# Optimization experiments

Measured on AMD Instinct MI355X. Metric: run time of the kernel, lower is better.

## Reference

```python
import jax, jax.numpy as jnp
import numpy as np

B, L, D_MODEL = 8, 1024, 1024
NUM_HEADS, QUERY_GROUPS = 16, 4
HEAD_DIM = D_MODEL // NUM_HEADS          # 64
HEADS_PER_GROUP = NUM_HEADS // QUERY_GROUPS
ROPE_THETA = 10000.0
QK_NORM_EPS = 1e-10
QKV_OUT = NUM_HEADS * HEAD_DIM + 2 * QUERY_GROUPS * HEAD_DIM  # 1536


def setup_inputs() -> dict:
    key = jax.random.key(0)
    k1, k2, k3 = jax.random.split(key, 3)
    x = jax.random.normal(k1, (B, L, D_MODEL), dtype=jnp.float32)
    w_qkv = jax.random.normal(k2, (QKV_OUT, D_MODEL), dtype=jnp.float32) * 0.02
    w_o = jax.random.normal(k3, (D_MODEL, D_MODEL), dtype=jnp.float32) * 0.02
    return {"x": x, "w_qkv": w_qkv, "w_o": w_o, "H_patch": 32, "W_patch": 32}


def _qk_norm(t, eps=QK_NORM_EPS):
    # L2 normalize over head_dim (qk_norm_type=2)
    return t / (jnp.linalg.norm(t, axis=-1, keepdims=True) + eps)


def _rope2d(t, H, W):
    # t: [B, L, nh, hd] with L == H*W
    b, _, nh, hd = t.shape
    inv_freq = 1.0 / ROPE_THETA ** (jnp.arange(0, hd, 2, dtype=jnp.float32) / hd)  # [hd/2]
    pos_h = jnp.arange(H, dtype=jnp.float32)
    pos_w = jnp.arange(W, dtype=jnp.float32)
    # additive combination of H and W frequencies: [H, W, hd/2]
    freqs = pos_h[:, None, None] * inv_freq + pos_w[None, :, None] * inv_freq
    cos = jnp.cos(freqs)[None, :, :, None, :]  # [1,H,W,1,hd/2]
    sin = jnp.sin(freqs)[None, :, :, None, :]
    ts = t.reshape(b, H, W, nh, hd)
    x1, x2 = ts[..., ::2], ts[..., 1::2]
    rot = jnp.concatenate([x1 * cos - x2 * sin, x1 * sin + x2 * cos], axis=-1)
    return rot.reshape(b, H * W, nh, hd)


def reference(x, w_qkv, w_o, H_patch, W_patch):
    b, l, _ = x.shape
    qkv = jnp.einsum('bld,ed->ble', x, w_qkv)  # [B, L, QKV_OUT]
    q, k, v = jnp.split(qkv, [NUM_HEADS * HEAD_DIM, NUM_HEADS * HEAD_DIM + QUERY_GROUPS * HEAD_DIM], axis=-1)
    q = q.reshape(b, l, NUM_HEADS, HEAD_DIM)
    k = k.reshape(b, l, QUERY_GROUPS, HEAD_DIM)
    v = v.reshape(b, l, QUERY_GROUPS, HEAD_DIM)
    # QK norm (use_qk_norm=True default)
    q = _qk_norm(q)
    k = _qk_norm(k)
    # 2D RoPE
    q = _rope2d(q, H_patch, W_patch)
    k = _rope2d(k, H_patch, W_patch)
    # GQA head expansion (use_mqa=False): repeat_interleave along head dim
    k = jnp.repeat(k, HEADS_PER_GROUP, axis=2)
    v = jnp.repeat(v, HEADS_PER_GROUP, axis=2)
    # [B, nh, L, hd]
    q = q.transpose(0, 2, 1, 3)
    k = k.transpose(0, 2, 1, 3)
    v = v.transpose(0, 2, 1, 3)
    # SDPA with default scale (softmax_scale arg is ignored by the original code);
    # padding_mask=None path: attn_mask ends up None, so no causal mask either.
    scale = 1.0 / jnp.sqrt(jnp.float32(HEAD_DIM))
    scores = jnp.einsum('bhqd,bhkd->bhqk', q, k) * scale
    attn = jax.nn.softmax(scores, axis=-1)
    out = jnp.einsum('bhqk,bhkd->bhqd', attn, v)
    out = out.transpose(0, 2, 1, 3).reshape(b, l, D_MODEL)
    return jnp.einsum('bld,ed->ble', out, w_o)
```

## Files before the change

kernel.cpp:

```cpp
#include <hip/hip_runtime.h>
#include <hip/hip_bf16.h>
#include <cstdint>
#include <cstddef>


typedef __bf16 bf16x8 __attribute__((ext_vector_type(8)));
typedef __bf16 bf16x4 __attribute__((ext_vector_type(4)));
typedef float floatx4 __attribute__((ext_vector_type(4)));
typedef uint32_t u32x2 __attribute__((ext_vector_type(2)));
typedef uint32_t u32x4 __attribute__((ext_vector_type(4)));

typedef unsigned int u32_g __attribute__((address_space(1)));
typedef unsigned int u32_l __attribute__((address_space(3)));

__device__ __forceinline__ void gl_lds16(const void* g, void* l) {
  __builtin_amdgcn_global_load_lds((const u32_g*)g, (u32_l*)l, 16, 0, 0);
}

constexpr int CH = 520;
__device__ __forceinline__ int pidx(int r, int k) {
  return (r >> 3) * CH + (r & 7) * 64 + k;
}

#define LOG2_THETA 13.287712379549449f

__global__ __launch_bounds__(256)
void cvt_all(const float* __restrict__ x, const float* __restrict__ wq,
             const float* __restrict__ wo, __bf16* __restrict__ out) {
  int i = blockIdx.x * 256 + threadIdx.x;
  float4 v;
  if (i < 2097152)      v = ((const float4*)x)[i];
  else if (i < 2490368) v = ((const float4*)wq)[i - 2097152];
  else                  v = ((const float4*)wo)[i - 2490368];
  bf16x4 o = {(__bf16)v.x, (__bf16)v.y, (__bf16)v.z, (__bf16)v.w};
  ((bf16x4*)out)[i] = o;
}

__global__ __launch_bounds__(256, 2)
void gemm_qkv(const __bf16* __restrict__ A, const __bf16* __restrict__ Bw,
              __bf16* __restrict__ Q, __bf16* __restrict__ Ko,
              __bf16* __restrict__ Vt, const int* __restrict__ Wp) {
  __shared__ __align__(16) __bf16 sAB[32 * CH];
  __bf16* sA = sAB;
  __bf16* sB = sAB + 16 * CH;
  const int tid = threadIdx.x, wave = tid >> 6, lane = tid & 63;
  const int quad = lane >> 4, lm = lane & 15;
  const int bm = blockIdx.x / 12, bn = blockIdx.x % 12;
  const int wm = wave & 1, wn = wave >> 1;
  const int rowA0 = bm << 7, rowB0 = bn << 7;
  const int lr = lane >> 3, lc = (lane & 7) * 8;

  floatx4 acc[4][4] = {};

  for (int k0 = 0; k0 < 1024; k0 += 64) {
    __syncthreads();
    for (int j = 0; j < 4; ++j) {
      int c = wave * 4 + j;
      gl_lds16(A + (size_t)(rowA0 + c * 8 + lr) * 1024 + k0 + lc, sA + c * CH);
      gl_lds16(Bw + (size_t)(rowB0 + c * 8 + lr) * 1024 + k0 + lc, sB + c * CH);
    }
    __syncthreads();
    for (int kb = 0; kb < 64; kb += 32) {
      const int ko = kb + quad * 8;
      bf16x8 af[4], bfv[4];
      for (int t = 0; t < 4; ++t) {
        af[t]  = *(const bf16x8*)(sA + pidx(wm * 64 + t * 16 + lm, ko));
        bfv[t] = *(const bf16x8*)(sB + pidx(wn * 64 + t * 16 + lm, ko));
      }
      for (int mt = 0; mt < 4; ++mt)
        for (int nt = 0; nt < 4; ++nt)
          acc[mt][nt] = __builtin_amdgcn_mfma_f32_16x16x32_bf16(af[mt], bfv[nt],
                                                                acc[mt][nt], 0, 0, 0);
    }
  }

  __syncthreads();

  const int hc = bn * 2 + wn;
  const int row0 = rowA0 + wm * 64;
  const int bb = row0 >> 10, l0 = row0 & 1023;

  if (hc < 20) {
    const bool isq = hc < 16;
    const int W = Wp[0];
    const float invfA = exp2f(-(float)lm * 0.03125f * LOG2_THETA);
    const float invfB = exp2f(-(float)(lm + 16) * 0.03125f * LOG2_THETA);
    __bf16* base = isq
        ? Q + (((size_t)bb * 16 + hc) * 1024 + l0) * 64
        : Ko + (((size_t)bb * 4 + (hc - 16)) * 1024 + l0) * 64;
    const int srcA = (lane & 48) | ((2 * lm) & 15);
    const bool lo = lm < 8;
    for (int mt = 0; mt < 4; ++mt)
      for (int r = 0; r < 4; ++r) {
        float a0 = acc[mt][0][r], a1 = acc[mt][1][r];
        float a2 = acc[mt][2][r], a3 = acc[mt][3][r];
        float ss = a0 * a0 + a1 * a1 + a2 * a2 + a3 * a3;
        ss += __shfl_xor(ss, 1); ss += __shfl_xor(ss, 2);
        ss += __shfl_xor(ss, 4); ss += __shfl_xor(ss, 8);
        float rn = (isq ? 0.125f : 1.0f) / (sqrtf(ss) + 1e-10f);
        a0 *= rn; a1 *= rn; a2 *= rn; a3 *= rn;
        float e0 = __shfl(a0, srcA),     e1 = __shfl(a1, srcA);
        float f0 = __shfl(a0, srcA + 1), f1 = __shfl(a1, srcA + 1);
        float g0 = __shfl(a2, srcA),     g1 = __shfl(a3, srcA);
        float h0 = __shfl(a2, srcA + 1), h1 = __shfl(a3, srcA + 1);
        float x1A = lo ? e0 : e1, x2A = lo ? f0 : f1;
        float x1B = lo ? g0 : g1, x2B = lo ? h0 : h1;
        int lrow = l0 + mt * 16 + quad * 4 + r;
        int pos = lrow / W + lrow % W;
        float fA = (float)pos * invfA, fB = (float)pos * invfB;
        float cA = __cosf(fA), sA_ = __sinf(fA);
        float cB = __cosf(fB), sB_ = __sinf(fB);
        __bf16* dst = base + (size_t)(mt * 16 + quad * 4 + r) * 64;
        dst[lm]      = (__bf16)(x1A * cA - x2A * sA_);
        dst[lm + 16] = (__bf16)(x1B * cB - x2B * sB_);
        dst[lm + 32] = (__bf16)(x1A * sA_ + x2A * cA);
        dst[lm + 48] = (__bf16)(x1B * sB_ + x2B * cB);
      }
  } else {
    const int g = hc - 20;
    __bf16* sT = sAB + wave * 4160;
    for (int mt = 0; mt < 4; ++mt)
      for (int nt = 0; nt < 4; ++nt)
        for (int r = 0; r < 4; ++r)
          sT[(mt * 16 + quad * 4 + r) * 65 + nt * 16 + lm] =
              (__bf16)acc[mt][nt][r];
    for (int pp = 0; pp < 8; ++pp) {
      int d = pp * 8 + (lane >> 3);
      int lloc = (lane & 7) * 8;
      bf16x8 o;
      for (int j = 0; j < 8; ++j) o[j] = sT[(lloc + j) * 65 + d];
      *(bf16x8*)(Vt + (((size_t)bb * 4 + g) * 64 + d) * 1024 + l0 + lloc) = o;
    }
  }
}

__global__ __launch_bounds__(256, 2)
void gemm_bt(const __bf16* __restrict__ A, const __bf16* __restrict__ B,
             float* __restrict__ Cf, int M, int N, int K) {
  __shared__ __align__(16) __bf16 sA[16 * CH];
  __shared__ __align__(16) __bf16 sB[16 * CH];
  const int tid = threadIdx.x;
  const int wave = tid >> 6, lane = tid & 63;
  const int ntiles = N >> 7;
  const int bm = blockIdx.x / ntiles, bn = blockIdx.x % ntiles;
  const int wm = wave & 1, wn = wave >> 1;
  const int rowA0 = bm << 7, rowB0 = bn << 7;
  const int lr = lane >> 3;
  const int lc = (lane & 7) * 8;

  floatx4 acc[4][4] = {};

  for (int k0 = 0; k0 < K; k0 += 64) {
    __syncthreads();
    for (int j = 0; j < 4; ++j) {
      int c = wave * 4 + j;
      gl_lds16(A + (size_t)(rowA0 + c * 8 + lr) * K + k0 + lc, sA + c * CH);
      gl_lds16(B + (size_t)(rowB0 + c * 8 + lr) * K + k0 + lc, sB + c * CH);
    }
    __syncthreads();
    for (int kb = 0; kb < 64; kb += 32) {
      const int ko = kb + (lane >> 4) * 8;
      bf16x8 af[4], bfv[4];
      for (int t = 0; t < 4; ++t) {
        af[t]  = *(const bf16x8*)(sA + pidx(wm * 64 + t * 16 + (lane & 15), ko));
        bfv[t] = *(const bf16x8*)(sB + pidx(wn * 64 + t * 16 + (lane & 15), ko));
      }
      for (int mt = 0; mt < 4; ++mt)
        for (int nt = 0; nt < 4; ++nt)
          acc[mt][nt] = __builtin_amdgcn_mfma_f32_16x16x32_bf16(af[mt], bfv[nt],
                                                                acc[mt][nt], 0, 0, 0);
    }
  }
  for (int mt = 0; mt < 4; ++mt)
    for (int nt = 0; nt < 4; ++nt)
      for (int r = 0; r < 4; ++r) {
        int row = rowA0 + wm * 64 + mt * 16 + (lane >> 4) * 4 + r;
        int col = rowB0 + wn * 64 + nt * 16 + (lane & 15);
        Cf[(size_t)row * N + col] = acc[mt][nt][r];
      }
}

__global__ __launch_bounds__(256, 4)
void flash(const __bf16* __restrict__ Q, const __bf16* __restrict__ K,
           const __bf16* __restrict__ Vt, __bf16* __restrict__ Oout) {
  __shared__ __align__(16) __bf16 sKV[16384];
  __shared__ float sL[128];
  const int tid = threadIdx.x, wave = tid >> 6, lane = tid & 63;
  const int quad = lane >> 4, lm = lane & 15;
  const int qt = blockIdx.x & 7, h = (blockIdx.x >> 3) & 15, b = blockIdx.x >> 7;
  const int g = h >> 2;
  const __bf16* Qb = Q + (((size_t)b * 16 + h) * 1024 + qt * 128) * 64;
  const __bf16* Kb = K + ((size_t)b * 4 + g) * 1024 * 64;
  const __bf16* Vb = Vt + ((size_t)b * 4 + g) * 64 * 1024;

  const int r8 = lane >> 3, gsw = (lane & 7) ^ r8;

  for (int j = 0; j < 4; ++j) {
    int c = wave * 4 + j;
    gl_lds16(Qb + (size_t)(c * 8 + r8) * 64 + gsw * 8, sKV + c * 512);
  }
  __syncthreads();
  bf16x8 qf[2][2];
  for (int mt = 0; mt < 2; ++mt)
    for (int hh = 0; hh < 2; ++hh) {
      int r = wave * 32 + mt * 16 + lm;
      qf[mt][hh] = *(const bf16x8*)(sKV + (r >> 3) * 512 + (r & 7) * 64 +
                                    (((hh * 4 + quad) ^ (r & 7)) * 8));
    }

  float l_acc[2] = {0.f, 0.f};
  floatx4 accO[2][4] = {};

  for (int kt = 0; kt < 8; ++kt) {
    __syncthreads();
    {
      int half = wave & 1;
      if (wave < 2) {
        for (int c = 0; c < 8; ++c)
          gl_lds16(Kb + (size_t)(kt * 128 + half * 64 + c * 8 + r8) * 64 + gsw * 8,
                   sKV + half * 4096 + c * 512);
      } else {
        for (int c = 0; c < 8; ++c)
          gl_lds16(Vb + (size_t)(c * 8 + r8) * 1024 + kt * 128 + half * 64 + gsw * 8,
                   sKV + 8192 + half * 4096 + c * 512);
      }
    }
    __syncthreads();

    for (int half = 0; half < 2; ++half) {
      const __bf16* sK = sKV + half * 4096;
      const __bf16* sV = sKV + 8192 + half * 4096;

      floatx4 accT[4][2] = {};
      for (int hh = 0; hh < 2; ++hh) {
        bf16x8 kf[4];
        for (int nt = 0; nt < 4; ++nt) {
          int r = nt * 16 + lm;
          kf[nt] = *(const bf16x8*)(sK + (r >> 3) * 512 + (r & 7) * 64 +
                                    (((hh * 4 + quad) ^ (r & 7)) * 8));
        }
        for (int nt = 0; nt < 4; ++nt)
          for (int mt = 0; mt < 2; ++mt)
            accT[nt][mt] = __builtin_amdgcn_mfma_f32_16x16x32_bf16(
                kf[nt], qf[mt][hh], accT[nt][mt], 0, 0, 0);
      }

      bf16x8 pf[2][2];
      for (int nt = 0; nt < 4; ++nt)
        for (int mt = 0; mt < 2; ++mt)
          for (int r = 0; r < 4; ++r) {
            float y = accT[nt][mt][r];
            float p = fmaf(y, fmaf(y, 0.5f, 1.0f), 1.0f);
            l_acc[mt] += p;
            pf[nt >> 1][mt][(nt & 1) * 4 + r] = (__bf16)p;
          }

      for (int hh = 0; hh < 2; ++hh)
        for (int dt = 0; dt < 4; ++dt) {
          int r = dt * 16 + lm;
          int rowoff = (r >> 3) * 512 + (r & 7) * 64;
          int lgA = hh * 4 + (quad >> 1);
          u32x2 vA = *(const u32x2*)(sV + rowoff + ((lgA ^ (r & 7)) * 8) + (quad & 1) * 4);
          u32x2 vB = *(const u32x2*)(sV + rowoff + (((lgA + 2) ^ (r & 7)) * 8) + (quad & 1) * 4);
          u32x4 vw = {vA[0], vA[1], vB[0], vB[1]};
          bf16x8 vf = __builtin_bit_cast(bf16x8, vw);
          for (int mt = 0; mt < 2; ++mt)
            accO[mt][dt] = __builtin_amdgcn_mfma_f32_16x16x32_bf16(
                pf[hh][mt], vf, accO[mt][dt], 0, 0, 0);
        }
    }
  }

  for (int mt = 0; mt < 2; ++mt) {
    float l = l_acc[mt];
    l += __shfl_xor(l, 16);
    l += __shfl_xor(l, 32);
    if (quad == 0) sL[wave * 32 + mt * 16 + lm] = l;
  }
  __syncthreads();

  for (int mt = 0; mt < 2; ++mt)
    for (int r = 0; r < 4; ++r) {
      float inv = 1.f / sL[wave * 32 + mt * 16 + quad * 4 + r];
      int row = qt * 128 + wave * 32 + mt * 16 + quad * 4 + r;
      for (int dt = 0; dt < 4; ++dt) {
        int col = dt * 16 + lm;
        Oout[((size_t)b * 1024 + row) * 1024 + h * 64 + col] =
            (__bf16)(accO[mt][dt][r] * inv);
      }
    }
}

extern "C" void kernel_launch(void* const* d_in, const int* in_sizes, int n_in,
                              void* d_out, int out_size, void* d_ws, size_t ws_size,
                              hipStream_t stream) {
  const float* x     = (const float*)d_in[0];
  const float* w_qkv = (const float*)d_in[1];
  const float* w_o   = (const float*)d_in[2];
  const int*   Wp    = (const int*)d_in[4];
  float* out = (float*)d_out;
  char* ws = (char*)d_ws;

  __bf16* xb    = (__bf16*)(ws + 0);
  __bf16* attn  = (__bf16*)(ws + 0);
  __bf16* wqkvb = (__bf16*)(ws + 16777216);
  __bf16* wob   = (__bf16*)(ws + 19922944);
  __bf16* Qb    = (__bf16*)(ws + 22020096);
  __bf16* Kb    = (__bf16*)(ws + 38797312);
  __bf16* Vtb   = (__bf16*)(ws + 42991616);

  cvt_all<<<10752, 256, 0, stream>>>(x, w_qkv, w_o, (__bf16*)ws);

  gemm_qkv<<<64 * 12, 256, 0, stream>>>(xb, wqkvb, Qb, Kb, Vtb, Wp);

  flash<<<1024, 256, 0, stream>>>(Qb, Kb, Vtb, attn);

  gemm_bt<<<64 * 8, 256, 0, stream>>>(attn, wob, out, 8192, 1024, 1024);
}
```

Measured before the change: 213.4 us.

## Enlarge flash query tile to 256 rows and use rotation-swizzled LDS layouts

```diff
diff --git a/kernel.cpp b/kernel.cpp
--- a/kernel.cpp
+++ b/kernel.cpp
@@ -17,9 +17,8 @@
   __builtin_amdgcn_global_load_lds((const u32_g*)g, (u32_l*)l, 16, 0, 0);
 }
 
-constexpr int CH = 520;
-__device__ __forceinline__ int pidx(int r, int k) {
-  return (r >> 3) * CH + (r & 7) * 64 + k;
+__device__ __forceinline__ int fidx8(int row, int g) {
+  return (row * 8 + ((g + row) & 7)) * 8;
 }
 
 #define LOG2_THETA 13.287712379549449f
@@ -40,15 +39,16 @@
 void gemm_qkv(const __bf16* __restrict__ A, const __bf16* __restrict__ Bw,
               __bf16* __restrict__ Q, __bf16* __restrict__ Ko,
               __bf16* __restrict__ Vt, const int* __restrict__ Wp) {
-  __shared__ __align__(16) __bf16 sAB[32 * CH];
+  __shared__ __align__(16) __bf16 sAB[16640];
   __bf16* sA = sAB;
-  __bf16* sB = sAB + 16 * CH;
+  __bf16* sB = sAB + 8192;
   const int tid = threadIdx.x, wave = tid >> 6, lane = tid & 63;
   const int quad = lane >> 4, lm = lane & 15;
   const int bm = blockIdx.x / 12, bn = blockIdx.x % 12;
   const int wm = wave & 1, wn = wave >> 1;
   const int rowA0 = bm << 7, rowB0 = bn << 7;
-  const int lr = lane >> 3, lc = (lane & 7) * 8;
+  const int r8 = lane >> 3;
+  const int gg = ((lane & 7) - r8) & 7;
 
   floatx4 acc[4][4] = {};
 
@@ -56,16 +56,16 @@
     __syncthreads();
     for (int j = 0; j < 4; ++j) {
       int c = wave * 4 + j;
-      gl_lds16(A + (size_t)(rowA0 + c * 8 + lr) * 1024 + k0 + lc, sA + c * CH);
-      gl_lds16(Bw + (size_t)(rowB0 + c * 8 + lr) * 1024 + k0 + lc, sB + c * CH);
+      gl_lds16(A + (size_t)(rowA0 + c * 8 + r8) * 1024 + k0 + gg * 8, sA + c * 512);
+      gl_lds16(Bw + (size_t)(rowB0 + c * 8 + r8) * 1024 + k0 + gg * 8, sB + c * 512);
     }
     __syncthreads();
     for (int kb = 0; kb < 64; kb += 32) {
-      const int ko = kb + quad * 8;
+      const int gk = (kb >> 3) + quad;
       bf16x8 af[4], bfv[4];
       for (int t = 0; t < 4; ++t) {
-        af[t]  = *(const bf16x8*)(sA + pidx(wm * 64 + t * 16 + lm, ko));
-        bfv[t] = *(const bf16x8*)(sB + pidx(wn * 64 + t * 16 + lm, ko));
+        af[t]  = *(const bf16x8*)(sA + fidx8(wm * 64 + t * 16 + lm, gk));
+        bfv[t] = *(const bf16x8*)(sB + fidx8(wn * 64 + t * 16 + lm, gk));
       }
       for (int mt = 0; mt < 4; ++mt)
         for (int nt = 0; nt < 4; ++nt)
@@ -137,16 +137,16 @@
 __global__ __launch_bounds__(256, 2)
 void gemm_bt(const __bf16* __restrict__ A, const __bf16* __restrict__ B,
              float* __restrict__ Cf, int M, int N, int K) {
-  __shared__ __align__(16) __bf16 sA[16 * CH];
-  __shared__ __align__(16) __bf16 sB[16 * CH];
+  __shared__ __align__(16) __bf16 sA[8192];
+  __shared__ __align__(16) __bf16 sB[8192];
   const int tid = threadIdx.x;
   const int wave = tid >> 6, lane = tid & 63;
   const int ntiles = N >> 7;
   const int bm = blockIdx.x / ntiles, bn = blockIdx.x % ntiles;
   const int wm = wave & 1, wn = wave >> 1;
   const int rowA0 = bm << 7, rowB0 = bn << 7;
-  const int lr = lane >> 3;
-  const int lc = (lane & 7) * 8;
+  const int r8 = lane >> 3;
+  const int gg = ((lane & 7) - r8) & 7;
 
   floatx4 acc[4][4] = {};
 
@@ -154,16 +154,16 @@
     __syncthreads();
     for (int j = 0; j < 4; ++j) {
       int c = wave * 4 + j;
-      gl_lds16(A + (size_t)(rowA0 + c * 8 + lr) * K + k0 + lc, sA + c * CH);
-      gl_lds16(B + (size_t)(rowB0 + c * 8 + lr) * K + k0 + lc, sB + c * CH);
+      gl_lds16(A + (size_t)(rowA0 + c * 8 + r8) * K + k0 + gg * 8, sA + c * 512);
+      gl_lds16(B + (size_t)(rowB0 + c * 8 + r8) * K + k0 + gg * 8, sB + c * 512);
     }
     __syncthreads();
     for (int kb = 0; kb < 64; kb += 32) {
-      const int ko = kb + (lane >> 4) * 8;
+      const int gk = (kb >> 3) + (lane >> 4);
       bf16x8 af[4], bfv[4];
       for (int t = 0; t < 4; ++t) {
-        af[t]  = *(const bf16x8*)(sA + pidx(wm * 64 + t * 16 + (lane & 15), ko));
-        bfv[t] = *(const bf16x8*)(sB + pidx(wn * 64 + t * 16 + (lane & 15), ko));
+        af[t]  = *(const bf16x8*)(sA + fidx8(wm * 64 + t * 16 + (lane & 15), gk));
+        bfv[t] = *(const bf16x8*)(sB + fidx8(wn * 64 + t * 16 + (lane & 15), gk));
       }
       for (int mt = 0; mt < 4; ++mt)
         for (int nt = 0; nt < 4; ++nt)
@@ -180,74 +180,64 @@
       }
 }
 
-__global__ __launch_bounds__(256, 4)
+__global__ __launch_bounds__(256, 2)
 void flash(const __bf16* __restrict__ Q, const __bf16* __restrict__ K,
            const __bf16* __restrict__ Vt, __bf16* __restrict__ Oout) {
   __shared__ __align__(16) __bf16 sKV[16384];
-  __shared__ float sL[128];
+  __shared__ float sL[256];
   const int tid = threadIdx.x, wave = tid >> 6, lane = tid & 63;
   const int quad = lane >> 4, lm = lane & 15;
-  const int qt = blockIdx.x & 7, h = (blockIdx.x >> 3) & 15, b = blockIdx.x >> 7;
+  const int qt = blockIdx.x & 3, h = (blockIdx.x >> 2) & 15, b = blockIdx.x >> 6;
   const int g = h >> 2;
-  const __bf16* Qb = Q + (((size_t)b * 16 + h) * 1024 + qt * 128) * 64;
+  const __bf16* Qb = Q + (((size_t)b * 16 + h) * 1024 + qt * 256) * 64;
   const __bf16* Kb = K + ((size_t)b * 4 + g) * 1024 * 64;
   const __bf16* Vb = Vt + ((size_t)b * 4 + g) * 64 * 1024;
 
-  const int r8 = lane >> 3, gsw = (lane & 7) ^ r8;
-
-  for (int j = 0; j < 4; ++j) {
-    int c = wave * 4 + j;
-    gl_lds16(Qb + (size_t)(c * 8 + r8) * 64 + gsw * 8, sKV + c * 512);
+  const int r8 = lane >> 3;
+  const int gg = ((lane & 7) - r8) & 7;
+  const int r16 = lane >> 4;
+
+  for (int j = 0; j < 8; ++j) {
+    int c = wave * 8 + j;
+    gl_lds16(Qb + (size_t)(c * 8 + r8) * 64 + gg * 8, sKV + c * 512);
   }
   __syncthreads();
-  bf16x8 qf[2][2];
-  for (int mt = 0; mt < 2; ++mt)
-    for (int hh = 0; hh < 2; ++hh) {
-      int r = wave * 32 + mt * 16 + lm;
-      qf[mt][hh] = *(const bf16x8*)(sKV + (r >> 3) * 512 + (r & 7) * 64 +
-                                    (((hh * 4 + quad) ^ (r & 7)) * 8));
-    }
-
-  float l_acc[2] = {0.f, 0.f};
-  floatx4 accO[2][4] = {};
+  bf16x8 qf[4][2];
+  for (int mt = 0; mt < 4; ++mt)
+    for (int hh = 0; hh < 2; ++hh)
+      qf[mt][hh] = *(const bf16x8*)(sKV + fidx8(wave * 64 + mt * 16 + lm,
+                                                hh * 4 + quad));
+
+  float l_acc[4] = {};
+  floatx4 accO[4][4] = {};
 
   for (int kt = 0; kt < 8; ++kt) {
     __syncthreads();
-    {
-      int half = wave & 1;
-      if (wave < 2) {
-        for (int c = 0; c < 8; ++c)
-          gl_lds16(Kb + (size_t)(kt * 128 + half * 64 + c * 8 + r8) * 64 + gsw * 8,
-                   sKV + half * 4096 + c * 512);
-      } else {
-        for (int c = 0; c < 8; ++c)
-          gl_lds16(Vb + (size_t)(c * 8 + r8) * 1024 + kt * 128 + half * 64 + gsw * 8,
-                   sKV + 8192 + half * 4096 + c * 512);
-      }
-    }
-    __syncthreads();
-
-    for (int half = 0; half < 2; ++half) {
-      const __bf16* sK = sKV + half * 4096;
-      const __bf16* sV = sKV + 8192 + half * 4096;
-
-      floatx4 accT[4][2] = {};
+    for (int j = 0; j < 4; ++j) {
+      int c = wave * 4 + j;
+      gl_lds16(Kb + (size_t)(kt * 128 + c * 8 + r8) * 64 + gg * 8, sKV + c * 512);
+      int d = c * 4 + r16;
+      int gv = ((lane & 15) - r16 - 4 * c) & 15;
+      gl_lds16(Vb + (size_t)d * 1024 + kt * 128 + gv * 8, sKV + 8192 + c * 512);
+    }
+    __syncthreads();
+
+    for (int h64 = 0; h64 < 2; ++h64) {
+      floatx4 accT[4][4] = {};
       for (int hh = 0; hh < 2; ++hh) {
         bf16x8 kf[4];
-        for (int nt = 0; nt < 4; ++nt) {
-          int r = nt * 16 + lm;
-          kf[nt] = *(const bf16x8*)(sK + (r >> 3) * 512 + (r & 7) * 64 +
-                                    (((hh * 4 + quad) ^ (r & 7)) * 8));
-        }
         for (int nt = 0; nt < 4; ++nt)
-          for (int mt = 0; mt < 2; ++mt)
+          kf[nt] = *(const bf16x8*)(sKV + fidx8(h64 * 64 + nt * 16 + lm,
+                                                hh * 4 + quad));
+        for (int nt = 0; nt < 4; ++nt)
+          for (int mt = 0; mt < 4; ++mt)
             accT[nt][mt] = __builtin_amdgcn_mfma_f32_16x16x32_bf16(
                 kf[nt], qf[mt][hh], accT[nt][mt], 0, 0, 0);
       }
 
-      bf16x8 pf[2][2];
+      bf16x8 pf[2][4];
       for (int nt = 0; nt < 4; ++nt)
-        for (int mt = 0; mt < 2; ++mt)
+        for (int mt = 0; mt < 4; ++mt)
           for (int r = 0; r < 4; ++r) {
             float y = accT[nt][mt][r];
             float p = fmaf(y, fmaf(y, 0.5f, 1.0f), 1.0f);
@@ -257,32 +247,34 @@
 
       for (int hh = 0; hh < 2; ++hh)
         for (int dt = 0; dt < 4; ++dt) {
-          int r = dt * 16 + lm;
-          int rowoff = (r >> 3) * 512 + (r & 7) * 64;
-          int lgA = hh * 4 + (quad >> 1);
-          u32x2 vA = *(const u32x2*)(sV + rowoff + ((lgA ^ (r & 7)) * 8) + (quad & 1) * 4);
-          u32x2 vB = *(const u32x2*)(sV + rowoff + (((lgA + 2) ^ (r & 7)) * 8) + (quad & 1) * 4);
+          int d = dt * 16 + lm;
+          int kgA = h64 * 8 + hh * 4 + (quad >> 1);
+          const __bf16* sV = sKV + 8192;
+          u32x2 vA = *(const u32x2*)(sV + (d * 16 + ((kgA + d) & 15)) * 8 +
+                                     (quad & 1) * 4);
+          u32x2 vB = *(const u32x2*)(sV + (d * 16 + ((kgA + 2 + d) & 15)) * 8 +
+                                     (quad & 1) * 4);
           u32x4 vw = {vA[0], vA[1], vB[0], vB[1]};
           bf16x8 vf = __builtin_bit_cast(bf16x8, vw);
-          for (int mt = 0; mt < 2; ++mt)
+          for (int mt = 0; mt < 4; ++mt)
             accO[mt][dt] = __builtin_amdgcn_mfma_f32_16x16x32_bf16(
                 pf[hh][mt], vf, accO[mt][dt], 0, 0, 0);
         }
     }
   }
 
-  for (int mt = 0; mt < 2; ++mt) {
+  for (int mt = 0; mt < 4; ++mt) {
     float l = l_acc[mt];
     l += __shfl_xor(l, 16);
     l += __shfl_xor(l, 32);
-    if (quad == 0) sL[wave * 32 + mt * 16 + lm] = l;
+    if (quad == 0) sL[wave * 64 + mt * 16 + lm] = l;
   }
   __syncthreads();
 
-  for (int mt = 0; mt < 2; ++mt)
+  for (int mt = 0; mt < 4; ++mt)
     for (int r = 0; r < 4; ++r) {
-      float inv = 1.f / sL[wave * 32 + mt * 16 + quad * 4 + r];
-      int row = qt * 128 + wave * 32 + mt * 16 + quad * 4 + r;
+      float inv = 1.f / sL[wave * 64 + mt * 16 + quad * 4 + r];
+      int row = qt * 256 + wave * 64 + mt * 16 + quad * 4 + r;
       for (int dt = 0; dt < 4; ++dt) {
         int col = dt * 16 + lm;
         Oout[((size_t)b * 1024 + row) * 1024 + h * 64 + col] =
@@ -313,7 +305,7 @@
 
   gemm_qkv<<<64 * 12, 256, 0, stream>>>(xb, wqkvb, Qb, Kb, Vtb, Wp);
 
-  flash<<<1024, 256, 0, stream>>>(Qb, Kb, Vtb, attn);
+  flash<<<512, 256, 0, stream>>>(Qb, Kb, Vtb, attn);
 
   gemm_bt<<<64 * 8, 256, 0, stream>>>(attn, wob, out, 8192, 1024, 1024);
 }
```

Measured after the change: 274.4 us. +28.5%, slower.
